# Kernel optimization log

Measured on AMD Instinct MI355X. Metric: run time of the kernel, lower is better.

## Reference

```python
import jax, jax.numpy as jnp
import numpy as np

HEADS = 8
D_K = 64
LN_EPS = 1e-6


def setup_inputs() -> dict:
    key = jax.random.key(0)
    ks = jax.random.split(key, 12)
    B, S, D = 4, 2048, 512
    inp = {
        "key": jax.random.normal(ks[0], (B, S, D), jnp.float32),
        "value": jax.random.normal(ks[1], (B, S, D), jnp.float32),
        "query": jax.random.normal(ks[2], (B, S, D), jnp.float32),
        "mask": jax.random.randint(ks[3], (B, S, S), 0, 2).astype(bool),
        # projection weights (torch Linear: y = x @ W.T + b)
        "Wk": jax.random.normal(ks[4], (D, D), jnp.float32) * (1.0 / np.sqrt(D)),
        "bk": jnp.zeros((D,), jnp.float32),
        "Wv": jax.random.normal(ks[5], (D, D), jnp.float32) * (1.0 / np.sqrt(D)),
        "bv": jnp.zeros((D,), jnp.float32),
        "Wq": jax.random.normal(ks[6], (D, D), jnp.float32) * (1.0 / np.sqrt(D)),
        "bq": jnp.zeros((D,), jnp.float32),
        # LayerNorm gain/bias
        "a2": jnp.ones((D,), jnp.float32),
        "b2": jnp.zeros((D,), jnp.float32),
    }
    return inp


def _attention(key, value, query, mask, Wk, bk, Wv, bv, Wq, bq, a2, b2):
    B, Sq, D = query.shape
    Sk = key.shape[1]
    H, dk = HEADS, D_K

    def split_heads(x, W, b):
        y = x @ W.T + b                                   # [B, S, D]
        return y.reshape(x.shape[0], x.shape[1], H, dk).transpose(0, 2, 1, 3)  # [B,H,S,dk]

    k_up = split_heads(key, Wk, bk)
    v_up = split_heads(value, Wv, bv)
    q_up = split_heads(query, Wq, bq)

    # scaled dot-product scores, full [B,H,Sq,Sk] matrix (as in the original bmm)
    scores = jnp.einsum("bhqd,bhkd->bhqk", q_up, k_up) / jnp.sqrt(jnp.asarray(dk, scores_dtype(q_up)))
    scores = jnp.where(mask[:, None, :, :], -jnp.inf, scores)
    attn = jax.nn.softmax(scores, axis=-1)                # dropout p=0 -> identity

    out = jnp.einsum("bhqk,bhkd->bhqd", attn, v_up)       # [B,H,Sq,dk]
    out = out.transpose(0, 2, 1, 3).reshape(B, Sq, D)
    res = out + query                                     # residual (res_dropout p=0)

    # OpenNMT LayerNorm: (x - mu) / (std + eps) * a2 + b2, unbiased std
    mu = res.mean(axis=-1, keepdims=True)
    var = jnp.sum((res - mu) ** 2, axis=-1, keepdims=True) / (D - 1)
    res = a2 * (res - mu) / (jnp.sqrt(var) + LN_EPS) + b2

    attn_flat = attn.reshape(B * H, Sq, Sk)               # matches torch [B*H, Sq, Sk]
    return res, attn_flat


def scores_dtype(x):
    return x.dtype


def reference(key, value, query, mask, Wk, bk, Wv, bv, Wq, bq, a2, b2):
    return _attention(key, value, query, mask, Wk, bk, Wv, bv, Wq, bq, a2, b2)
```

## Files before the change

kernel.cpp:

```cpp
#include <hip/hip_runtime.h>
#include <stdint.h>

typedef float f32x4 __attribute__((ext_vector_type(4)));
typedef short bf16x8 __attribute__((ext_vector_type(8)));

constexpr int NB = 4;
constexpr int NS = 2048;
constexpr int ND = 512;
constexpr int NH = 8;
constexpr int NDK = 64;
constexpr int NT = NS / 64;
constexpr float QSCALE = 0.125f * 1.44269504088896340736f;

static __device__ __forceinline__ unsigned short f2bf(float f) {
    union { float f; uint32_t u; } v; v.f = f;
    uint32_t r = (v.u + 0x7FFFu + ((v.u >> 16) & 1u)) >> 16;
    return (unsigned short)r;
}
static __device__ __forceinline__ unsigned short f2bf_fast(float f) {
    union { float f; uint32_t u; } v; v.f = f;
    return (unsigned short)((v.u + 0x8000u) >> 16);
}
static __device__ __forceinline__ float exp2_fast(float x) {
#if __has_builtin(__builtin_amdgcn_exp2f)
    return __builtin_amdgcn_exp2f(x);
#else
    return exp2f(x);
#endif
}

static __device__ __forceinline__ void gload_lds16(const void* g, void* l) {
    __builtin_amdgcn_global_load_lds((const __attribute__((address_space(1))) void*)g,
                                     (__attribute__((address_space(3))) void*)l, 16, 0, 0);
}

__global__ __launch_bounds__(256) void cvt3_kernel(const float4* __restrict__ a,
                                                   const float4* __restrict__ b,
                                                   const float4* __restrict__ c,
                                                   ushort4* __restrict__ oa,
                                                   ushort4* __restrict__ ob,
                                                   ushort4* __restrict__ oc, int n4) {
    int which = blockIdx.y;
    const float4* in = which == 0 ? a : which == 1 ? b : c;
    ushort4* out = which == 0 ? oa : which == 1 ? ob : oc;
    int i = blockIdx.x * blockDim.x + threadIdx.x;
    if (i >= n4) return;
    float4 v = in[i];
    ushort4 o;
    o.x = f2bf(v.x); o.y = f2bf(v.y); o.z = f2bf(v.z); o.w = f2bf(v.w);
    out[i] = o;
}

__global__ __launch_bounds__(256) void bitmask_kernel(const int* __restrict__ mask,
                                                      unsigned long long* __restrict__ bm,
                                                      int nwords) {
    int lane = threadIdx.x & 63;
    int wave = threadIdx.x >> 6;
    int wgid = blockIdx.x * 4 + wave;
    int nw = gridDim.x * 4;
    for (int c = wgid; c < nwords; c += nw) {
        int v = mask[(size_t)c * 64 + lane];
        unsigned long long bits = __ballot(v != 0);
        if (lane == 0) bm[c] = bits;
    }
}

__global__ __launch_bounds__(256) void proj_kernel(const unsigned short* __restrict__ xq,
                                                   const unsigned short* __restrict__ xk,
                                                   const unsigned short* __restrict__ xv,
                                                   const unsigned short* __restrict__ wq,
                                                   const unsigned short* __restrict__ wk,
                                                   const unsigned short* __restrict__ wv,
                                                   const float* __restrict__ bq,
                                                   const float* __restrict__ bk,
                                                   const float* __restrict__ bv,
                                                   unsigned short* __restrict__ Qw,
                                                   unsigned short* __restrict__ Kw,
                                                   unsigned short* __restrict__ VTw) {
    int z = blockIdx.z;
    const unsigned short* X = z == 0 ? xq : z == 1 ? xk : xv;
    const unsigned short* W = z == 0 ? wq : z == 1 ? wk : wv;
    const float* bias = z == 0 ? bq : z == 1 ? bk : bv;
    unsigned short* out = z == 0 ? Qw : z == 1 ? Kw : VTw;
    float scale = z == 0 ? QSCALE : 1.0f;
    int vtrans = (z == 2);

    int lane = threadIdx.x & 63;
    int wave = threadIdx.x >> 6;
    int lrow = lane & 15, lgrp = lane >> 4;
    int m0 = blockIdx.x * 64 + wave * 16;
    int n0 = blockIdx.y * 64;

    f32x4 acc[4] = {{0.f,0.f,0.f,0.f},{0.f,0.f,0.f,0.f},{0.f,0.f,0.f,0.f},{0.f,0.f,0.f,0.f}};
    const unsigned short* xrow = X + (size_t)(m0 + lrow) * ND;
    for (int k = 0; k < ND; k += 32) {
        bf16x8 a = *(const bf16x8*)(xrow + k + lgrp * 8);
#pragma unroll
        for (int n = 0; n < 4; n++) {
            bf16x8 b = *(const bf16x8*)(W + (size_t)(n0 + n * 16 + lrow) * ND + k + lgrp * 8);
            acc[n] = __builtin_amdgcn_mfma_f32_16x16x32_bf16(a, b, acc[n], 0, 0, 0);
        }
    }
#pragma unroll
    for (int n = 0; n < 4; n++) {
        int col = n0 + n * 16 + lrow;
        int h = col >> 6, d = col & 63;
        float bv_ = bias[col];
#pragma unroll
        for (int j = 0; j < 4; j++) {
            int m = m0 + lgrp * 4 + j;
            int bidx = m >> 11, s = m & (NS - 1);
            float y = (acc[n][j] + bv_) * scale;
            size_t off = vtrans ? ((size_t)(bidx * NH + h) * NDK + d) * NS + s
                                : ((size_t)(bidx * NH + h) * NS + s) * NDK + d;
            out[off] = f2bf(y);
        }
    }
}

__global__ __launch_bounds__(512) void attn_kernel(const unsigned short* __restrict__ Q,
                                                   const unsigned short* __restrict__ K,
                                                   const unsigned short* __restrict__ VT,
                                                   const unsigned long long* __restrict__ bm,
                                                   float* __restrict__ attn_out,
                                                   float* __restrict__ Ob) {
    __shared__ __align__(16) unsigned short kb[2][64 * 64];
    __shared__ __align__(16) unsigned short vb[2][64 * 64];
    __shared__ __align__(16) unsigned short pl[8][16][80];

    int lane = threadIdx.x & 63;
    int wave = threadIdx.x >> 6;
    int lrow = lane & 15, lgrp = lane >> 4;

    int id = blockIdx.x;
    int xcd = id & 7;
    int loc = id >> 3;
    int bh = xcd * 4 + (loc >> 4);
    int qb = loc & 15;
    int b = bh >> 3, h = bh & 7;
    int qw = qb * 128 + wave * 16;

    const unsigned short* qrow = Q + ((size_t)bh * NS + qw + lrow) * NDK + lgrp * 8;
    bf16x8 aq0 = *(const bf16x8*)(qrow);
    bf16x8 aq1 = *(const bf16x8*)(qrow + 32);

    const unsigned short* kbase = K + (size_t)bh * NS * NDK;
    const unsigned short* vbase = VT + (size_t)bh * NDK * NS;
    const unsigned long long* bmb = bm + (size_t)b * NS * (NS / 64);
    int bmoff[4];
#pragma unroll
    for (int j = 0; j < 4; j++) bmoff[j] = (qw + lgrp * 4 + j) * (NS / 64);

    int rl = lane >> 3, cc = lane & 7;
    int cs = (cc ^ rl) * 8;

    {
        const unsigned short* s0 = kbase + (size_t)(8 * wave + rl) * NDK + cs;
        gload_lds16(s0, &kb[0][wave * 512]);
    }
    unsigned long long wc[4], wn[4];
#pragma unroll
    for (int j = 0; j < 4; j++) wc[j] = bmb[bmoff[j]];
    asm volatile("s_waitcnt vmcnt(0)" ::: "memory");
    __builtin_amdgcn_s_barrier();

    float lacc[4] = {0.f, 0.f, 0.f, 0.f};
    for (int t = 0; t < NT; t++) {
        int buf = t & 1;
        int tn = (t + 1 < NT) ? t + 1 : t;
        if (t + 1 < NT) {
            const unsigned short* s0 = kbase + (size_t)(tn * 64 + 8 * wave + rl) * NDK + cs;
            gload_lds16(s0, &kb[buf ^ 1][wave * 512]);
        }
#pragma unroll
        for (int j = 0; j < 4; j++) wn[j] = bmb[bmoff[j] + tn];

        f32x4 sc[4] = {{0.f,0.f,0.f,0.f},{0.f,0.f,0.f,0.f},{0.f,0.f,0.f,0.f},{0.f,0.f,0.f,0.f}};
        __builtin_amdgcn_s_setprio(1);
#pragma unroll
        for (int n = 0; n < 4; n++) {
            int R = n * 16 + lrow;
            bf16x8 b0 = *(const bf16x8*)&kb[buf][R * 64 + ((lgrp ^ (lrow & 7)) * 8)];
            bf16x8 b1 = *(const bf16x8*)&kb[buf][R * 64 + (((4 + lgrp) ^ (lrow & 7)) * 8)];
            sc[n] = __builtin_amdgcn_mfma_f32_16x16x32_bf16(aq0, b0, sc[n], 0, 0, 0);
            sc[n] = __builtin_amdgcn_mfma_f32_16x16x32_bf16(aq1, b1, sc[n], 0, 0, 0);
        }
        __builtin_amdgcn_s_setprio(0);
#pragma unroll
        for (int j = 0; j < 4; j++) {
            uint32_t wlo = (uint32_t)wc[j], whi = (uint32_t)(wc[j] >> 32);
#pragma unroll
            for (int n = 0; n < 4; n++) {
                uint32_t bit = ((n < 2 ? wlo : whi) >> ((n & 1) * 16 + lrow)) & 1u;
                float e = exp2_fast(sc[n][j]);
                lacc[j] += bit ? 0.f : e;
            }
        }
#pragma unroll
        for (int j = 0; j < 4; j++) wc[j] = wn[j];
        if (t + 1 < NT) {
            asm volatile("s_waitcnt vmcnt(0)" ::: "memory");
            __builtin_amdgcn_s_barrier();
        }
    }
    float li[4];
#pragma unroll
    for (int j = 0; j < 4; j++) {
        float l = lacc[j];
        l += __shfl_xor(l, 1);
        l += __shfl_xor(l, 2);
        l += __shfl_xor(l, 4);
        l += __shfl_xor(l, 8);
        li[j] = -__log2f(l);
    }

    {
        const unsigned short* s0 = kbase + (size_t)(8 * wave + rl) * NDK + cs;
        gload_lds16(s0, &kb[0][wave * 512]);
        const unsigned short* s1 = vbase + (size_t)(8 * wave + rl) * NS + cs;
        gload_lds16(s1, &vb[0][wave * 512]);
    }
#pragma unroll
    for (int j = 0; j < 4; j++) wc[j] = bmb[bmoff[j]];
    asm volatile("s_waitcnt vmcnt(0)" ::: "memory");
    __builtin_amdgcn_s_barrier();

    f32x4 accO[4] = {{0.f,0.f,0.f,0.f},{0.f,0.f,0.f,0.f},{0.f,0.f,0.f,0.f},{0.f,0.f,0.f,0.f}};
    float* aout = attn_out + (size_t)bh * NS * NS;
    float* abase[4];
#pragma unroll
    for (int j = 0; j < 4; j++) abase[j] = aout + (size_t)(qw + lgrp * 4 + j) * NS + lrow;

    for (int t = 0; t < NT; t++) {
        int buf = t & 1;
        int kt = t * 64;
        int tn = (t + 1 < NT) ? t + 1 : t;
        if (t + 1 < NT) {
            const unsigned short* s0 = kbase + (size_t)(tn * 64 + 8 * wave + rl) * NDK + cs;
            gload_lds16(s0, &kb[buf ^ 1][wave * 512]);
            const unsigned short* s1 = vbase + (size_t)(8 * wave + rl) * NS + tn * 64 + cs;
            gload_lds16(s1, &vb[buf ^ 1][wave * 512]);
        }
#pragma unroll
        for (int j = 0; j < 4; j++) wn[j] = bmb[bmoff[j] + tn];

        f32x4 sc[4] = {{0.f,0.f,0.f,0.f},{0.f,0.f,0.f,0.f},{0.f,0.f,0.f,0.f},{0.f,0.f,0.f,0.f}};
        __builtin_amdgcn_s_setprio(1);
#pragma unroll
        for (int n = 0; n < 4; n++) {
            int R = n * 16 + lrow;
            bf16x8 b0 = *(const bf16x8*)&kb[buf][R * 64 + ((lgrp ^ (lrow & 7)) * 8)];
            bf16x8 b1 = *(const bf16x8*)&kb[buf][R * 64 + (((4 + lgrp) ^ (lrow & 7)) * 8)];
            sc[n] = __builtin_amdgcn_mfma_f32_16x16x32_bf16(aq0, b0, sc[n], 0, 0, 0);
            sc[n] = __builtin_amdgcn_mfma_f32_16x16x32_bf16(aq1, b1, sc[n], 0, 0, 0);
        }
        __builtin_amdgcn_s_setprio(0);
#pragma unroll
        for (int j = 0; j < 4; j++) {
            uint32_t wlo = (uint32_t)wc[j], whi = (uint32_t)(wc[j] >> 32);
#pragma unroll
            for (int n = 0; n < 4; n++) {
                uint32_t bit = ((n < 2 ? wlo : whi) >> ((n & 1) * 16 + lrow)) & 1u;
                float p = bit ? 0.f : exp2_fast(sc[n][j] + li[j]);
                abase[j][kt + n * 16] = p;
                pl[wave][lgrp * 4 + j][n * 16 + lrow] = f2bf_fast(p);
            }
        }
        __builtin_amdgcn_s_setprio(1);
#pragma unroll
        for (int step = 0; step < 2; step++) {
            bf16x8 ap = *(const bf16x8*)&pl[wave][lrow][step * 32 + lgrp * 8];
#pragma unroll
            for (int n = 0; n < 4; n++) {
                int R = n * 16 + lrow;
                bf16x8 bv = *(const bf16x8*)&vb[buf][R * 64 + (((4 * step + lgrp) ^ (lrow & 7)) * 8)];
                accO[n] = __builtin_amdgcn_mfma_f32_16x16x32_bf16(ap, bv, accO[n], 0, 0, 0);
            }
        }
        __builtin_amdgcn_s_setprio(0);
#pragma unroll
        for (int j = 0; j < 4; j++) wc[j] = wn[j];
        if (t + 1 < NT) {
            asm volatile("s_waitcnt vmcnt(16)" ::: "memory");
            __builtin_amdgcn_s_barrier();
        }
    }

#pragma unroll
    for (int n = 0; n < 4; n++)
#pragma unroll
        for (int j = 0; j < 4; j++) {
            int qi = qw + lgrp * 4 + j;
            Ob[((size_t)b * NS + qi) * ND + h * NDK + n * 16 + lrow] = accO[n][j];
        }
}

__global__ __launch_bounds__(256) void ln_kernel(const float* __restrict__ Ob,
                                                 const float* __restrict__ query,
                                                 const float* __restrict__ a2,
                                                 const float* __restrict__ b2,
                                                 float* __restrict__ out) {
    int row = blockIdx.x * 4 + (threadIdx.x >> 6);
    int lane = threadIdx.x & 63;
    const float4* orow = (const float4*)(Ob + (size_t)row * ND);
    const float4* qrow = (const float4*)(query + (size_t)row * ND);
    float4 v[2];
    float sum = 0.f;
#pragma unroll
    for (int t = 0; t < 2; t++) {
        float4 o = orow[lane + t * 64];
        float4 q = qrow[lane + t * 64];
        v[t].x = o.x + q.x; v[t].y = o.y + q.y; v[t].z = o.z + q.z; v[t].w = o.w + q.w;
        sum += v[t].x + v[t].y + v[t].z + v[t].w;
    }
#pragma unroll
    for (int s = 1; s < 64; s <<= 1) sum += __shfl_xor(sum, s);
    float mu = sum * (1.f / ND);
    float sq = 0.f;
#pragma unroll
    for (int t = 0; t < 2; t++) {
        float dx = v[t].x - mu, dy = v[t].y - mu, dz = v[t].z - mu, dw = v[t].w - mu;
        sq += dx * dx + dy * dy + dz * dz + dw * dw;
    }
#pragma unroll
    for (int s = 1; s < 64; s <<= 1) sq += __shfl_xor(sq, s);
    float var = sq * (1.f / (ND - 1));
    float inv = 1.f / (sqrtf(var) + 1e-6f);
    float4* orow_out = (float4*)(out + (size_t)row * ND);
#pragma unroll
    for (int t = 0; t < 2; t++) {
        float4 g = ((const float4*)a2)[lane + t * 64];
        float4 bb = ((const float4*)b2)[lane + t * 64];
        float4 r;
        r.x = g.x * (v[t].x - mu) * inv + bb.x;
        r.y = g.y * (v[t].y - mu) * inv + bb.y;
        r.z = g.z * (v[t].z - mu) * inv + bb.z;
        r.w = g.w * (v[t].w - mu) * inv + bb.w;
        orow_out[lane + t * 64] = r;
    }
}

extern "C" void kernel_launch(void* const* d_in, const int* in_sizes, int n_in,
                              void* d_out, int out_size, void* d_ws, size_t ws_size,
                              hipStream_t stream) {
    const float* key   = (const float*)d_in[0];
    const float* value = (const float*)d_in[1];
    const float* query = (const float*)d_in[2];
    const int*   mask  = (const int*)d_in[3];
    const float* Wk = (const float*)d_in[4];
    const float* bk = (const float*)d_in[5];
    const float* Wv = (const float*)d_in[6];
    const float* bv = (const float*)d_in[7];
    const float* Wq = (const float*)d_in[8];
    const float* bq = (const float*)d_in[9];
    const float* a2 = (const float*)d_in[10];
    const float* b2 = (const float*)d_in[11];

    const size_t nX = (size_t)NB * NS * ND;
    const size_t nW = (size_t)ND * ND;
    const int    nBMw = NB * NS * NS / 64;

    unsigned short* xq  = (unsigned short*)d_ws;
    unsigned short* xk  = xq + nX;
    unsigned short* xv  = xk + nX;
    unsigned short* wqb = xv + nX;
    unsigned short* wkb = wqb + nW;
    unsigned short* wvb = wkb + nW;
    unsigned short* Qw  = wvb + nW;
    unsigned short* Kw  = Qw + nX;
    unsigned short* VTw = Kw + nX;
    float* Ow = (float*)(VTw + nX);
    unsigned long long* bmw = (unsigned long long*)(Ow + nX);

    bitmask_kernel<<<2048, 256, 0, stream>>>(mask, bmw, nBMw);

    cvt3_kernel<<<dim3((int)(nX / 4 / 256), 3), 256, 0, stream>>>(
        (const float4*)query, (const float4*)key, (const float4*)value,
        (ushort4*)xq, (ushort4*)xk, (ushort4*)xv, (int)(nX / 4));
    cvt3_kernel<<<dim3((int)(nW / 4 / 256), 3), 256, 0, stream>>>(
        (const float4*)Wq, (const float4*)Wk, (const float4*)Wv,
        (ushort4*)wqb, (ushort4*)wkb, (ushort4*)wvb, (int)(nW / 4));

    proj_kernel<<<dim3(128, 8, 3), 256, 0, stream>>>(xq, xk, xv, wqb, wkb, wvb,
                                                     bq, bk, bv, Qw, Kw, VTw);

    float* attn_out = (float*)d_out + nX;
    attn_kernel<<<512, 512, 0, stream>>>(Qw, Kw, VTw, bmw, attn_out, Ow);

    ln_kernel<<<2048, 256, 0, stream>>>(Ow, query, a2, b2, (float*)d_out);
}
```

Baseline: 360.1 us.

## Transpose score MFMA so each lane owns a query row, vectorize attn stores

Swaps the MFMA operand order so each lane holds four consecutive key columns for one query row. That lets the attention-probability output be written as 16-byte nontemporal vector stores instead of scalar strided stores. The P tile is now packed as two bf16 pairs and written to LDS with one 8-byte store, and its row padding is reduced. Mask words drop from four 64-bit loads per tile to one per lane, and the row-sum reduction shrinks to two cross-lane shuffles. The vmcnt waits are retuned to match the fewer outstanding loads, which risks a hazard if the counts are wrong.

Result: no change. 362.7 us (+0.7%).

```diff
diff --git a/kernel.cpp b/kernel.cpp
--- a/kernel.cpp
+++ b/kernel.cpp
@@ -17,9 +17,9 @@
     uint32_t r = (v.u + 0x7FFFu + ((v.u >> 16) & 1u)) >> 16;
     return (unsigned short)r;
 }
-static __device__ __forceinline__ unsigned short f2bf_fast(float f) {
-    union { float f; uint32_t u; } v; v.f = f;
-    return (unsigned short)((v.u + 0x8000u) >> 16);
+static __device__ __forceinline__ uint32_t pkbf(float a, float b) {
+    union { float f; uint32_t u; } x, y; x.f = a; y.f = b;
+    return ((x.u + 0x8000u) >> 16) | (((y.u + 0x8000u) >> 16) << 16);
 }
 static __device__ __forceinline__ float exp2_fast(float x) {
 #if __has_builtin(__builtin_amdgcn_exp2f)
@@ -126,7 +126,7 @@
                                                    float* __restrict__ Ob) {
     __shared__ __align__(16) unsigned short kb[2][64 * 64];
     __shared__ __align__(16) unsigned short vb[2][64 * 64];
-    __shared__ __align__(16) unsigned short pl[8][16][80];
+    __shared__ __align__(16) unsigned short pl[8][16][72];
 
     int lane = threadIdx.x & 63;
     int wave = threadIdx.x >> 6;
@@ -146,35 +146,24 @@
 
     const unsigned short* kbase = K + (size_t)bh * NS * NDK;
     const unsigned short* vbase = VT + (size_t)bh * NDK * NS;
-    const unsigned long long* bmb = bm + (size_t)b * NS * (NS / 64);
-    int bmoff[4];
-#pragma unroll
-    for (int j = 0; j < 4; j++) bmoff[j] = (qw + lgrp * 4 + j) * (NS / 64);
+    const unsigned long long* bmrow = bm + ((size_t)b * NS + qw + lrow) * (NS / 64);
 
     int rl = lane >> 3, cc = lane & 7;
     int cs = (cc ^ rl) * 8;
 
-    {
-        const unsigned short* s0 = kbase + (size_t)(8 * wave + rl) * NDK + cs;
-        gload_lds16(s0, &kb[0][wave * 512]);
-    }
-    unsigned long long wc[4], wn[4];
-#pragma unroll
-    for (int j = 0; j < 4; j++) wc[j] = bmb[bmoff[j]];
-    asm volatile("s_waitcnt vmcnt(0)" ::: "memory");
+    gload_lds16(kbase + (size_t)(8 * wave + rl) * NDK + cs, &kb[0][wave * 512]);
+    unsigned long long wc = bmrow[0], wn = 0;
+    asm volatile("s_waitcnt vmcnt(1)" ::: "memory");
     __builtin_amdgcn_s_barrier();
 
-    float lacc[4] = {0.f, 0.f, 0.f, 0.f};
+    float lacc = 0.f;
     for (int t = 0; t < NT; t++) {
         int buf = t & 1;
-        int tn = (t + 1 < NT) ? t + 1 : t;
         if (t + 1 < NT) {
-            const unsigned short* s0 = kbase + (size_t)(tn * 64 + 8 * wave + rl) * NDK + cs;
-            gload_lds16(s0, &kb[buf ^ 1][wave * 512]);
-        }
-#pragma unroll
-        for (int j = 0; j < 4; j++) wn[j] = bmb[bmoff[j] + tn];
-
+            gload_lds16(kbase + (size_t)((t + 1) * 64 + 8 * wave + rl) * NDK + cs,
+                        &kb[buf ^ 1][wave * 512]);
+            wn = bmrow[t + 1];
+        }
         f32x4 sc[4] = {{0.f,0.f,0.f,0.f},{0.f,0.f,0.f,0.f},{0.f,0.f,0.f,0.f},{0.f,0.f,0.f,0.f}};
         __builtin_amdgcn_s_setprio(1);
 #pragma unroll
@@ -182,68 +171,48 @@
             int R = n * 16 + lrow;
             bf16x8 b0 = *(const bf16x8*)&kb[buf][R * 64 + ((lgrp ^ (lrow & 7)) * 8)];
             bf16x8 b1 = *(const bf16x8*)&kb[buf][R * 64 + (((4 + lgrp) ^ (lrow & 7)) * 8)];
-            sc[n] = __builtin_amdgcn_mfma_f32_16x16x32_bf16(aq0, b0, sc[n], 0, 0, 0);
-            sc[n] = __builtin_amdgcn_mfma_f32_16x16x32_bf16(aq1, b1, sc[n], 0, 0, 0);
+            sc[n] = __builtin_amdgcn_mfma_f32_16x16x32_bf16(b0, aq0, sc[n], 0, 0, 0);
+            sc[n] = __builtin_amdgcn_mfma_f32_16x16x32_bf16(b1, aq1, sc[n], 0, 0, 0);
         }
         __builtin_amdgcn_s_setprio(0);
-#pragma unroll
-        for (int j = 0; j < 4; j++) {
-            uint32_t wlo = (uint32_t)wc[j], whi = (uint32_t)(wc[j] >> 32);
-#pragma unroll
-            for (int n = 0; n < 4; n++) {
-                uint32_t bit = ((n < 2 ? wlo : whi) >> ((n & 1) * 16 + lrow)) & 1u;
+        uint32_t wlo = (uint32_t)wc, whi = (uint32_t)(wc >> 32);
+#pragma unroll
+        for (int n = 0; n < 4; n++)
+#pragma unroll
+            for (int j = 0; j < 4; j++) {
+                uint32_t bit = ((n < 2 ? wlo : whi) >> ((n & 1) * 16 + lgrp * 4 + j)) & 1u;
                 float e = exp2_fast(sc[n][j]);
-                lacc[j] += bit ? 0.f : e;
+                lacc += bit ? 0.f : e;
             }
-        }
-#pragma unroll
-        for (int j = 0; j < 4; j++) wc[j] = wn[j];
+        wc = wn;
         if (t + 1 < NT) {
-            asm volatile("s_waitcnt vmcnt(0)" ::: "memory");
+            asm volatile("s_waitcnt vmcnt(1)" ::: "memory");
             __builtin_amdgcn_s_barrier();
         }
     }
-    float li[4];
-#pragma unroll
-    for (int j = 0; j < 4; j++) {
-        float l = lacc[j];
-        l += __shfl_xor(l, 1);
-        l += __shfl_xor(l, 2);
-        l += __shfl_xor(l, 4);
-        l += __shfl_xor(l, 8);
-        li[j] = -__log2f(l);
-    }
-
-    {
-        const unsigned short* s0 = kbase + (size_t)(8 * wave + rl) * NDK + cs;
-        gload_lds16(s0, &kb[0][wave * 512]);
-        const unsigned short* s1 = vbase + (size_t)(8 * wave + rl) * NS + cs;
-        gload_lds16(s1, &vb[0][wave * 512]);
-    }
-#pragma unroll
-    for (int j = 0; j < 4; j++) wc[j] = bmb[bmoff[j]];
-    asm volatile("s_waitcnt vmcnt(0)" ::: "memory");
+    lacc += __shfl_xor(lacc, 16);
+    lacc += __shfl_xor(lacc, 32);
+    float li = -__log2f(lacc);
+
+    gload_lds16(kbase + (size_t)(8 * wave + rl) * NDK + cs, &kb[0][wave * 512]);
+    gload_lds16(vbase + (size_t)(8 * wave + rl) * NS + cs, &vb[0][wave * 512]);
+    wc = bmrow[0];
+    asm volatile("s_waitcnt vmcnt(1)" ::: "memory");
     __builtin_amdgcn_s_barrier();
 
     f32x4 accO[4] = {{0.f,0.f,0.f,0.f},{0.f,0.f,0.f,0.f},{0.f,0.f,0.f,0.f},{0.f,0.f,0.f,0.f}};
-    float* aout = attn_out + (size_t)bh * NS * NS;
-    float* abase[4];
-#pragma unroll
-    for (int j = 0; j < 4; j++) abase[j] = aout + (size_t)(qw + lgrp * 4 + j) * NS + lrow;
+    float* arow = attn_out + (size_t)bh * NS * NS + (size_t)(qw + lrow) * NS;
 
     for (int t = 0; t < NT; t++) {
         int buf = t & 1;
         int kt = t * 64;
-        int tn = (t + 1 < NT) ? t + 1 : t;
         if (t + 1 < NT) {
-            const unsigned short* s0 = kbase + (size_t)(tn * 64 + 8 * wave + rl) * NDK + cs;
-            gload_lds16(s0, &kb[buf ^ 1][wave * 512]);
-            const unsigned short* s1 = vbase + (size_t)(8 * wave + rl) * NS + tn * 64 + cs;
-            gload_lds16(s1, &vb[buf ^ 1][wave * 512]);
-        }
-#pragma unroll
-        for (int j = 0; j < 4; j++) wn[j] = bmb[bmoff[j] + tn];
-
+            gload_lds16(kbase + (size_t)((t + 1) * 64 + 8 * wave + rl) * NDK + cs,
+                        &kb[buf ^ 1][wave * 512]);
+            gload_lds16(vbase + (size_t)(8 * wave + rl) * NS + (t + 1) * 64 + cs,
+                        &vb[buf ^ 1][wave * 512]);
+            wn = bmrow[t + 1];
+        }
         f32x4 sc[4] = {{0.f,0.f,0.f,0.f},{0.f,0.f,0.f,0.f},{0.f,0.f,0.f,0.f},{0.f,0.f,0.f,0.f}};
         __builtin_amdgcn_s_setprio(1);
 #pragma unroll
@@ -251,20 +220,24 @@
             int R = n * 16 + lrow;
             bf16x8 b0 = *(const bf16x8*)&kb[buf][R * 64 + ((lgrp ^ (lrow & 7)) * 8)];
             bf16x8 b1 = *(const bf16x8*)&kb[buf][R * 64 + (((4 + lgrp) ^ (lrow & 7)) * 8)];
-            sc[n] = __builtin_amdgcn_mfma_f32_16x16x32_bf16(aq0, b0, sc[n], 0, 0, 0);
-            sc[n] = __builtin_amdgcn_mfma_f32_16x16x32_bf16(aq1, b1, sc[n], 0, 0, 0);
+            sc[n] = __builtin_amdgcn_mfma_f32_16x16x32_bf16(b0, aq0, sc[n], 0, 0, 0);
+            sc[n] = __builtin_amdgcn_mfma_f32_16x16x32_bf16(b1, aq1, sc[n], 0, 0, 0);
         }
         __builtin_amdgcn_s_setprio(0);
-#pragma unroll
-        for (int j = 0; j < 4; j++) {
-            uint32_t wlo = (uint32_t)wc[j], whi = (uint32_t)(wc[j] >> 32);
-#pragma unroll
-            for (int n = 0; n < 4; n++) {
-                uint32_t bit = ((n < 2 ? wlo : whi) >> ((n & 1) * 16 + lrow)) & 1u;
-                float p = bit ? 0.f : exp2_fast(sc[n][j] + li[j]);
-                abase[j][kt + n * 16] = p;
-                pl[wave][lgrp * 4 + j][n * 16 + lrow] = f2bf_fast(p);
-            }
+        uint32_t wlo = (uint32_t)wc, whi = (uint32_t)(wc >> 32);
+#pragma unroll
+        for (int n = 0; n < 4; n++) {
+            float p0, p1, p2, p3;
+            uint32_t wsel = (n < 2) ? wlo : whi;
+            int base = (n & 1) * 16 + lgrp * 4;
+            p0 = ((wsel >> (base + 0)) & 1u) ? 0.f : exp2_fast(sc[n][0] + li);
+            p1 = ((wsel >> (base + 1)) & 1u) ? 0.f : exp2_fast(sc[n][1] + li);
+            p2 = ((wsel >> (base + 2)) & 1u) ? 0.f : exp2_fast(sc[n][2] + li);
+            p3 = ((wsel >> (base + 3)) & 1u) ? 0.f : exp2_fast(sc[n][3] + li);
+            f32x4 pv4 = {p0, p1, p2, p3};
+            __builtin_nontemporal_store(pv4, (f32x4*)(arow + kt + n * 16 + lgrp * 4));
+            uint2 pk = {pkbf(p0, p1), pkbf(p2, p3)};
+            *(uint2*)&pl[wave][lrow][n * 16 + lgrp * 4] = pk;
         }
         __builtin_amdgcn_s_setprio(1);
 #pragma unroll
@@ -278,10 +251,9 @@
             }
         }
         __builtin_amdgcn_s_setprio(0);
-#pragma unroll
-        for (int j = 0; j < 4; j++) wc[j] = wn[j];
+        wc = wn;
         if (t + 1 < NT) {
-            asm volatile("s_waitcnt vmcnt(16)" ::: "memory");
+            asm volatile("s_waitcnt vmcnt(5)" ::: "memory");
             __builtin_amdgcn_s_barrier();
         }
     }
```
